# Optimization experiments

Measured on AMD Instinct MI355X. Metric: run time of the kernel, lower is better.

The kernel has to match this reference:

```python
import jax, jax.numpy as jnp
import numpy as np
import math

B = 16384
INPUT = 2048
HIDDEN = 2048
PROJ = 1024


def setup_inputs() -> dict:
    key = jax.random.key(0)
    ks = jax.random.split(key, 20)
    stdv = 1.0 / math.sqrt(PROJ)
    u = lambda k, shape: jax.random.uniform(k, shape, jnp.float32, -stdv, stdv)
    return {
        "x_t": jax.random.normal(ks[0], (B, INPUT), jnp.float32),
        "h_t": jax.random.normal(ks[1], (B, PROJ), jnp.float32),
        "c_t": jax.random.normal(ks[2], (B, HIDDEN), jnp.float32),
        "weight_if_x": u(ks[3], (INPUT, 2 * HIDDEN)),
        "weight_if_h": u(ks[4], (PROJ, 2 * HIDDEN)),
        "weight_if_c": u(ks[5], (HIDDEN, 2 * HIDDEN)),
        "bias_i": u(ks[6], (HIDDEN,)),
        "bias_f": u(ks[7], (HIDDEN,)),
        "weight_c_x": u(ks[8], (INPUT, HIDDEN)),
        "weight_c_h": u(ks[9], (PROJ, HIDDEN)),
        "bias_c": u(ks[10], (HIDDEN,)),
        "weight_o_x": u(ks[11], (INPUT, PROJ)),
        "weight_o_h": u(ks[12], (PROJ, PROJ)),
        "weight_o_c": u(ks[13], (HIDDEN, PROJ)),
        "bias_o": u(ks[14], (PROJ,)),
        "weight_r_proj": u(ks[15], (HIDDEN, PROJ)),
        "weight_r_x": u(ks[16], (INPUT, PROJ)),
    }


def reference(x_t, h_t, c_t, weight_if_x, weight_if_h, weight_if_c, bias_i, bias_f,
              weight_c_x, weight_c_h, bias_c, weight_o_x, weight_o_h, weight_o_c,
              bias_o, weight_r_proj, weight_r_x):
    # input/forget gates with peephole on c_t: [B, 2*HIDDEN]
    if_gates = x_t @ weight_if_x + h_t @ weight_if_h + c_t @ weight_if_c
    ingate, forgetgate = jnp.split(if_gates, 2, axis=-1)
    ingate = jax.nn.sigmoid(ingate + bias_i)
    forgetgate = jax.nn.sigmoid(forgetgate + bias_f)
    cellgate = jnp.tanh(x_t @ weight_c_x + h_t @ weight_c_h + bias_c)
    c_new = forgetgate * c_t + ingate * cellgate
    # output gate peeps at new cell state
    outgate = jax.nn.sigmoid(x_t @ weight_o_x + h_t @ weight_o_h + c_new @ weight_o_c + bias_o)
    r_t = jnp.tanh(c_new)
    m_t = r_t @ weight_r_proj
    # input_size != proj_size -> project x for the residual connection
    h_new = outgate * (m_t + x_t @ weight_r_x)
    return (h_new, c_new)
```

## Files before the change

### kernel.cpp

```cpp
#include <hip/hip_runtime.h>
#include <hip/hip_bf16.h>
#include <math.h>

typedef unsigned short u16;
typedef __bf16 bf16x8_t __attribute__((ext_vector_type(8)));
typedef float  f32x4_t  __attribute__((ext_vector_type(4)));
typedef float  f32x8_t  __attribute__((ext_vector_type(8)));
typedef u16    u16x4_t  __attribute__((ext_vector_type(4)));
typedef u16    u16x8_t  __attribute__((ext_vector_type(8)));

__device__ __forceinline__ u16 f2b(float f) {
  unsigned u = __builtin_bit_cast(unsigned, f);
  u += 0x7fffu + ((u >> 16) & 1u);
  return (u16)(u >> 16);
}
__device__ __forceinline__ float b2f(u16 h) {
  unsigned u = ((unsigned)h) << 16;
  return __builtin_bit_cast(float, u);
}
__device__ __forceinline__ float sigm_(float x) { return 1.0f / (1.0f + __expf(-x)); }
__device__ __forceinline__ float tanh_(float x) { return 1.0f - 2.0f / (__expf(2.0f * x) + 1.0f); }

__device__ __forceinline__ void gload16(const void* g, void* l) {
  __builtin_amdgcn_global_load_lds(
      (__attribute__((address_space(1))) void*)(g),
      (__attribute__((address_space(3))) void*)(l), 16, 0, 0);
}


__global__ void pack_act_kernel(const float* __restrict__ x, const float* __restrict__ h,
                                const float* __restrict__ c, u16* __restrict__ A1p) {
  int mb = blockIdx.x, kt = blockIdx.y, t = threadIdx.x;
  const float* src; int C, ccol;
  if (kt < 64)      { src = x; C = 2048; ccol = kt * 32; }
  else if (kt < 96) { src = h; C = 1024; ccol = (kt - 64) * 32; }
  else              { src = c; C = 2048; ccol = (kt - 96) * 32; }
  const float* s = src + (long)(mb * 256 + t) * C + ccol;
  u16* d = A1p + ((long)(mb * 160 + kt)) * 8192 + t * 8;
#pragma unroll
  for (int p = 0; p < 4; ++p) {
    f32x8_t v = *(const f32x8_t*)(s + p * 8);
    u16x8_t o;
#pragma unroll
    for (int r = 0; r < 8; ++r) o[r] = f2b(v[r]);
    *(u16x8_t*)(d + p * 2048) = o;
  }
}

__global__ void pack_w1_kernel(const float* __restrict__ w_if_x, const float* __restrict__ w_if_h,
                               const float* __restrict__ w_if_c, const float* __restrict__ w_c_x,
                               const float* __restrict__ w_c_h,  const float* __restrict__ w_o_x,
                               const float* __restrict__ w_o_h,  const float* __restrict__ w_r_x,
                               u16* __restrict__ W1tp) {
  int nb = blockIdx.x, kt = blockIdx.y, t = threadIdx.x;
  int n0g = nb * 256;
  const float* src; int N, nl, kl;
  if (n0g < 4096) {
    N = 4096; nl = n0g;
    if (kt < 64)      { src = w_if_x; kl = kt * 32; }
    else if (kt < 96) { src = w_if_h; kl = (kt - 64) * 32; }
    else              { src = w_if_c; kl = (kt - 96) * 32; }
  } else if (n0g < 6144) {
    N = 2048; nl = n0g - 4096;
    if (kt < 64)      { src = w_c_x; kl = kt * 32; }
    else if (kt < 96) { src = w_c_h; kl = (kt - 64) * 32; }
    else return;
  } else if (n0g < 7168) {
    N = 1024; nl = n0g - 6144;
    if (kt < 64)      { src = w_o_x; kl = kt * 32; }
    else if (kt < 96) { src = w_o_h; kl = (kt - 64) * 32; }
    else return;
  } else {
    N = 1024; nl = n0g - 7168;
    if (kt < 64)      { src = w_r_x; kl = kt * 32; }
    else return;
  }
  int n = nl + t;
  float tmp[32];
#pragma unroll
  for (int kk = 0; kk < 32; ++kk)
    tmp[kk] = src[(long)(kl + kk) * N + n];
  u16* d = W1tp + ((long)(nb * 160 + kt)) * 8192 + t * 8;
#pragma unroll
  for (int p = 0; p < 4; ++p) {
    u16x8_t o;
#pragma unroll
    for (int r = 0; r < 8; ++r) o[r] = f2b(tmp[p * 8 + r]);
    *(u16x8_t*)(d + p * 2048) = o;
  }
}

__global__ void pack_w2_kernel(const float* __restrict__ w_o_c,
                               const float* __restrict__ w_r_proj, u16* __restrict__ W2q) {
  int cg = blockIdx.x, kt = blockIdx.y, t = threadIdx.x;
  const float* src; int kl;
  if (kt < 64) { src = w_o_c;    kl = kt * 32; }
  else         { src = w_r_proj; kl = (kt - 64) * 32; }
  int n = cg * 128 + t;
  float tmp[32];
#pragma unroll
  for (int kk = 0; kk < 32; ++kk)
    tmp[kk] = src[(long)(kl + kk) * 1024 + n];
  u16* d = W2q + ((long)(cg * 128 + kt)) * 4096 + t * 8;
#pragma unroll
  for (int p = 0; p < 4; ++p) {
    u16x8_t o;
#pragma unroll
    for (int r = 0; r < 8; ++r) o[r] = f2b(tmp[p * 8 + r]);
    *(u16x8_t*)(d + p * 1024) = o;
  }
}

__global__ __launch_bounds__(512, 2) void gemm1_kernel(
    const u16* __restrict__ A, const u16* __restrict__ Bt, u16* __restrict__ Cout) {
  constexpr int KTF  = 160;
  constexpr int NCOL = 8192;
  constexpr int NBN  = 32;
  constexpr int SLOT = 16384;

  __shared__ u16 lds[3 * SLOT];

  int bid = blockIdx.x;
  int cpx = gridDim.x >> 3;
  bid = (bid & 7) * cpx + (bid >> 3);

  int mb = bid / NBN, nb = bid % NBN;
  int m0 = mb * 256, n0 = nb * 256;

  int NT = (nb < 16) ? 160 : ((nb < 28) ? 96 : 64);

  const int tid  = threadIdx.x;
  const int lane = tid & 63;
  const int wid  = tid >> 6;
  const int wr   = wid >> 2;
  const int wc   = wid & 3;
  const int hl16 = lane >> 4;
  const int l15  = lane & 15;

  const int dstg = tid * 8;
  const u16* pA = A  + ((long)(mb * KTF)) * 8192 + dstg;
  const u16* pB = Bt + ((long)(nb * KTF)) * 8192 + dstg;

#define STAGE(t, s) do { \
    gload16(pA + (long)(t) * 8192,        &lds[(s) * SLOT + dstg]); \
    gload16(pA + (long)(t) * 8192 + 4096, &lds[(s) * SLOT + dstg + 4096]); \
    gload16(pB + (long)(t) * 8192,        &lds[(s) * SLOT + 8192 + dstg]); \
    gload16(pB + (long)(t) * 8192 + 4096, &lds[(s) * SLOT + 8192 + dstg + 4096]); } while (0)

  const int aoff = hl16 * 2048 + (wr * 128 + l15) * 8;
  const int boff = hl16 * 2048 + (wc * 64  + l15) * 8;

  f32x4_t acc[8][4];
#pragma unroll
  for (int m = 0; m < 8; ++m)
#pragma unroll
    for (int n = 0; n < 4; ++n) acc[m][n] = (f32x4_t){0.f, 0.f, 0.f, 0.f};

  STAGE(0, 0); STAGE(1, 1);
  asm volatile("s_waitcnt vmcnt(4)" ::: "memory");
  __builtin_amdgcn_s_barrier();

  int slot = 0, s2 = 2;
  for (int t = 0; t < NT; ++t) {
    const u16* sA = &lds[slot * SLOT];
    const u16* sB = sA + 8192;
    const bool pre = (t + 2 < NT);
    if (pre) STAGE(t + 2, s2);

    bf16x8_t bv[4], av[8];
#pragma unroll
    for (int n = 0; n < 4; ++n) bv[n] = *(const bf16x8_t*)&sB[boff + n * 128];
#pragma unroll
    for (int m = 0; m < 8; ++m) av[m] = *(const bf16x8_t*)&sA[aoff + m * 128];

    __builtin_amdgcn_s_setprio(1);
#pragma unroll
    for (int m = 0; m < 8; ++m)
#pragma unroll
      for (int n = 0; n < 4; ++n)
        acc[m][n] = __builtin_amdgcn_mfma_f32_16x16x32_bf16(bv[n], av[m], acc[m][n], 0, 0, 0);
    __builtin_amdgcn_s_setprio(0);

    if (pre) asm volatile("s_waitcnt vmcnt(4)" ::: "memory");
    else     asm volatile("s_waitcnt vmcnt(0)" ::: "memory");
    __builtin_amdgcn_s_barrier();

    slot = (slot == 2) ? 0 : slot + 1;
    s2   = (s2   == 2) ? 0 : s2   + 1;
  }
#undef STAGE

  const int rowm = lane & 15;
  const int col4 = (lane >> 4) * 4;
#pragma unroll
  for (int m = 0; m < 8; ++m) {
    long rg = (long)(m0 + wr * 128 + m * 16 + rowm) * NCOL;
#pragma unroll
    for (int n = 0; n < 4; ++n) {
      int cg = n0 + wc * 64 + n * 16 + col4;
      u16x4_t o;
#pragma unroll
      for (int r = 0; r < 4; ++r) o[r] = f2b(acc[m][n][r]);
      *(u16x4_t*)&Cout[rg + cg] = o;
    }
  }
}

__global__ void pass2_kernel(const u16* __restrict__ G1, const float* __restrict__ c_t,
                             const float* __restrict__ bias_i, const float* __restrict__ bias_f,
                             const float* __restrict__ bias_c,
                             float* __restrict__ c_new_out, u16* __restrict__ A2p) {
  int mb = blockIdx.x, jg = blockIdx.y, t = threadIdx.x;
  int b = mb * 256 + t;
  int j0 = jg * 32;
  const u16* row = G1 + (long)b * 8192 + j0;
  const float* cp_p = c_t + (long)b * 2048 + j0;
  float* co_p = c_new_out + (long)b * 2048 + j0;
  u16* dc = A2p + ((long)(mb * 128 + jg)) * 8192 + t * 8;
  u16* dr = dc + (long)64 * 8192;

#pragma unroll
  for (int q = 0; q < 4; ++q) {
    u16x8_t ip = *(const u16x8_t*)(row + q * 8);
    u16x8_t fp = *(const u16x8_t*)(row + 2048 + q * 8);
    u16x8_t gp = *(const u16x8_t*)(row + 4096 + q * 8);
    f32x8_t cp = *(const f32x8_t*)(cp_p + q * 8);
    f32x8_t bi = *(const f32x8_t*)(bias_i + j0 + q * 8);
    f32x8_t bf = *(const f32x8_t*)(bias_f + j0 + q * 8);
    f32x8_t bc = *(const f32x8_t*)(bias_c + j0 + q * 8);
    f32x8_t cn;
    u16x8_t cb, rb;
#pragma unroll
    for (int r = 0; r < 8; ++r) {
      float ig = sigm_(b2f(ip[r]) + bi[r]);
      float fg = sigm_(b2f(fp[r]) + bf[r]);
      float g  = tanh_(b2f(gp[r]) + bc[r]);
      float c  = fg * cp[r] + ig * g;
      cn[r] = c;
      cb[r] = f2b(c);
      rb[r] = f2b(tanh_(c));
    }
    *(f32x8_t*)(co_p + q * 8) = cn;
    *(u16x8_t*)(dc + q * 2048) = cb;
    *(u16x8_t*)(dr + q * 2048) = rb;
  }
}

__global__ __launch_bounds__(512, 2) void gemm2h_kernel(
    const u16* __restrict__ A2p, const u16* __restrict__ W2q,
    const u16* __restrict__ G1, const float* __restrict__ bias_o,
    float* __restrict__ h_out) {
  constexpr int SLOT = 12288;

  __shared__ u16 lds[3 * SLOT];

  int bid = blockIdx.x;
  int cpx = gridDim.x >> 3;
  bid = (bid & 7) * cpx + (bid >> 3);

  int mb = bid >> 3, cg = bid & 7;
  int m0 = mb * 256, c0 = cg * 128;

  const int tid  = threadIdx.x;
  const int lane = tid & 63;
  const int wid  = tid >> 6;
  const int wr   = wid >> 1;
  const int wc   = wid & 1;
  const int hl16 = lane >> 4;
  const int l15  = lane & 15;

  const int dstg = tid * 8;
  const u16* pA = A2p + ((long)(mb * 128)) * 8192 + dstg;
  const u16* pB = W2q + ((long)(cg * 128)) * 4096 + dstg;

#define STAGE2(t, s) do { \
    gload16(pA + (long)(t) * 8192,        &lds[(s) * SLOT + dstg]); \
    gload16(pA + (long)(t) * 8192 + 4096, &lds[(s) * SLOT + dstg + 4096]); \
    gload16(pB + (long)(t) * 4096,        &lds[(s) * SLOT + 8192 + dstg]); } while (0)

  const int aoff = hl16 * 2048 + (wr * 64 + l15) * 8;
  const int boff = hl16 * 1024 + (wc * 64 + l15) * 8;

  f32x4_t acc0[4][4], acc1[4][4];
#pragma unroll
  for (int m = 0; m < 4; ++m)
#pragma unroll
    for (int n = 0; n < 4; ++n) {
      acc0[m][n] = (f32x4_t){0.f, 0.f, 0.f, 0.f};
      acc1[m][n] = (f32x4_t){0.f, 0.f, 0.f, 0.f};
    }

  STAGE2(0, 0); STAGE2(1, 1);
  asm volatile("s_waitcnt vmcnt(3)" ::: "memory");
  __builtin_amdgcn_s_barrier();

  int slot = 0, s2 = 2;
  for (int t = 0; t < 128; ++t) {
    const u16* sA = &lds[slot * SLOT];
    const u16* sB = sA + 8192;
    const bool pre = (t + 2 < 128);
    if (pre) STAGE2(t + 2, s2);

    bf16x8_t wv[4], av[4];
#pragma unroll
    for (int n = 0; n < 4; ++n) wv[n] = *(const bf16x8_t*)&sB[boff + n * 128];
#pragma unroll
    for (int m = 0; m < 4; ++m) av[m] = *(const bf16x8_t*)&sA[aoff + m * 128];

    __builtin_amdgcn_s_setprio(1);
    if (t < 64) {
#pragma unroll
      for (int m = 0; m < 4; ++m)
#pragma unroll
        for (int n = 0; n < 4; ++n)
          acc0[m][n] = __builtin_amdgcn_mfma_f32_16x16x32_bf16(wv[n], av[m], acc0[m][n], 0, 0, 0);
    } else {
#pragma unroll
      for (int m = 0; m < 4; ++m)
#pragma unroll
        for (int n = 0; n < 4; ++n)
          acc1[m][n] = __builtin_amdgcn_mfma_f32_16x16x32_bf16(wv[n], av[m], acc1[m][n], 0, 0, 0);
    }
    __builtin_amdgcn_s_setprio(0);

    if (pre) asm volatile("s_waitcnt vmcnt(3)" ::: "memory");
    else     asm volatile("s_waitcnt vmcnt(0)" ::: "memory");
    __builtin_amdgcn_s_barrier();

    slot = (slot == 2) ? 0 : slot + 1;
    s2   = (s2   == 2) ? 0 : s2   + 1;
  }
#undef STAGE2

#pragma unroll
  for (int m = 0; m < 4; ++m) {
    int row = m0 + wr * 64 + m * 16 + l15;
    const u16* g1r = G1 + (long)row * 8192;
#pragma unroll
    for (int n = 0; n < 4; ++n) {
      int jb = c0 + wc * 64 + n * 16 + 4 * hl16;
      u16x4_t og = *(const u16x4_t*)(g1r + 6144 + jb);
      u16x4_t xr = *(const u16x4_t*)(g1r + 7168 + jb);
      f32x4_t bo = *(const f32x4_t*)(bias_o + jb);
      f32x4_t h;
#pragma unroll
      for (int r = 0; r < 4; ++r) {
        float ogate = sigm_(acc0[m][n][r] + b2f(og[r]) + bo[r]);
        h[r] = ogate * (acc1[m][n][r] + b2f(xr[r]));
      }
      *(f32x4_t*)&h_out[(long)row * 1024 + jb] = h;
    }
  }
}

extern "C" void kernel_launch(void* const* d_in, const int* in_sizes, int n_in,
                              void* d_out, int out_size, void* d_ws, size_t ws_size,
                              hipStream_t stream) {
  const float* x_t      = (const float*)d_in[0];
  const float* h_t      = (const float*)d_in[1];
  const float* c_t      = (const float*)d_in[2];
  const float* w_if_x   = (const float*)d_in[3];
  const float* w_if_h   = (const float*)d_in[4];
  const float* w_if_c   = (const float*)d_in[5];
  const float* bias_i   = (const float*)d_in[6];
  const float* bias_f   = (const float*)d_in[7];
  const float* w_c_x    = (const float*)d_in[8];
  const float* w_c_h    = (const float*)d_in[9];
  const float* bias_c   = (const float*)d_in[10];
  const float* w_o_x    = (const float*)d_in[11];
  const float* w_o_h    = (const float*)d_in[12];
  const float* w_o_c    = (const float*)d_in[13];
  const float* bias_o   = (const float*)d_in[14];
  const float* w_r_proj = (const float*)d_in[15];
  const float* w_r_x    = (const float*)d_in[16];

  char* ws = (char*)d_ws;
  u16* A1p  = (u16*)(ws);
  u16* W1tp = (u16*)(ws + 167772160L);
  u16* G1   = (u16*)(ws + 251658240L);
  u16* W2q  = (u16*)(ws + 520093696L);
  u16* A2p  = (u16*)(ws);

  float* h_out = (float*)d_out;
  float* c_out = h_out + 16384L * 1024L;

  pack_act_kernel<<<dim3(64, 160), 256, 0, stream>>>(x_t, h_t, c_t, A1p);
  pack_w1_kernel<<<dim3(32, 160), 256, 0, stream>>>(w_if_x, w_if_h, w_if_c, w_c_x, w_c_h,
                                                    w_o_x, w_o_h, w_r_x, W1tp);
  pack_w2_kernel<<<dim3(8, 128), 128, 0, stream>>>(w_o_c, w_r_proj, W2q);

  gemm1_kernel<<<2048, 512, 0, stream>>>(A1p, W1tp, G1);

  pass2_kernel<<<dim3(64, 64), 256, 0, stream>>>(G1, c_t, bias_i, bias_f, bias_c, c_out, A2p);

  gemm2h_kernel<<<512, 512, 0, stream>>>(A2p, W2q, G1, bias_o, h_out);
}
```

Baseline: 1.492 ms.

## Software-pipeline LDS fragment reads with a 4-slot ring and double-buffered registers

The GEMM main loop moves from a 3-slot to a 4-slot LDS ring and issues global-to-LDS staging three tiles ahead. The loop is unrolled by two with ping-pong register fragment sets, so half of the next tile's operands are read from LDS while the current tile's MFMAs run. The goal is to hide LDS read latency behind matrix-core work instead of stalling before each MFMA burst. In exchange it uses more LDS and more registers, and the wait count still only lets one staged tile stay outstanding, which limits how much extra global-load overlap is gained.

```diff
diff --git a/kernel.cpp b/kernel.cpp
--- a/kernel.cpp
+++ b/kernel.cpp
@@ -111,6 +111,8 @@
   }
 }
 
+struct FragSet { bf16x8_t bv[4]; bf16x8_t av[4]; };
+
 __global__ __launch_bounds__(512, 2) void gemm1_kernel(
     const u16* __restrict__ A, const u16* __restrict__ Bt, u16* __restrict__ Cout) {
   constexpr int KTF  = 160;
@@ -118,7 +120,7 @@
   constexpr int NBN  = 32;
   constexpr int SLOT = 16384;
 
-  __shared__ u16 lds[3 * SLOT];
+  __shared__ u16 lds[4 * SLOT];
 
   int bid = blockIdx.x;
   int cpx = gridDim.x >> 3;
@@ -150,45 +152,64 @@
   const int aoff = hl16 * 2048 + (wr * 128 + l15) * 8;
   const int boff = hl16 * 2048 + (wc * 64  + l15) * 8;
 
+#define RD_P(S, si) do { \
+    const u16* _pb = &lds[(si) * SLOT]; \
+    const u16* _pc = _pb + 8192; \
+    _Pragma("unroll") \
+    for (int n = 0; n < 4; ++n) S.bv[n] = *(const bf16x8_t*)&_pc[boff + n * 128]; \
+    _Pragma("unroll") \
+    for (int m = 0; m < 4; ++m) S.av[m] = *(const bf16x8_t*)&_pb[aoff + m * 128]; } while (0)
+
+#define ITER(TT, P, N) do { \
+    const int _t = (TT); \
+    const u16* _sb = &lds[(_t & 3) * SLOT]; \
+    if (_t + 3 < NT) STAGE(_t + 3, (_t + 3) & 3); \
+    bf16x8_t _aq0 = *(const bf16x8_t*)&_sb[aoff + 4 * 128]; \
+    bf16x8_t _aq1 = *(const bf16x8_t*)&_sb[aoff + 5 * 128]; \
+    bf16x8_t _aq2 = *(const bf16x8_t*)&_sb[aoff + 6 * 128]; \
+    bf16x8_t _aq3 = *(const bf16x8_t*)&_sb[aoff + 7 * 128]; \
+    __builtin_amdgcn_s_setprio(1); \
+    _Pragma("unroll") \
+    for (int m = 0; m < 4; ++m) \
+      _Pragma("unroll") \
+      for (int n = 0; n < 4; ++n) \
+        acc[m][n] = __builtin_amdgcn_mfma_f32_16x16x32_bf16(P.bv[n], P.av[m], acc[m][n], 0, 0, 0); \
+    __builtin_amdgcn_s_setprio(0); \
+    if (_t + 1 < NT) RD_P(N, (_t + 1) & 3); \
+    __builtin_amdgcn_s_setprio(1); \
+    _Pragma("unroll") \
+    for (int n = 0; n < 4; ++n) { \
+      acc[4][n] = __builtin_amdgcn_mfma_f32_16x16x32_bf16(P.bv[n], _aq0, acc[4][n], 0, 0, 0); \
+      acc[5][n] = __builtin_amdgcn_mfma_f32_16x16x32_bf16(P.bv[n], _aq1, acc[5][n], 0, 0, 0); \
+      acc[6][n] = __builtin_amdgcn_mfma_f32_16x16x32_bf16(P.bv[n], _aq2, acc[6][n], 0, 0, 0); \
+      acc[7][n] = __builtin_amdgcn_mfma_f32_16x16x32_bf16(P.bv[n], _aq3, acc[7][n], 0, 0, 0); \
+    } \
+    __builtin_amdgcn_s_setprio(0); \
+    if (_t + 3 < NT) asm volatile("s_waitcnt vmcnt(4)" ::: "memory"); \
+    else             asm volatile("s_waitcnt vmcnt(0)" ::: "memory"); \
+    __builtin_amdgcn_s_barrier(); \
+  } while (0)
+
   f32x4_t acc[8][4];
 #pragma unroll
   for (int m = 0; m < 8; ++m)
 #pragma unroll
     for (int n = 0; n < 4; ++n) acc[m][n] = (f32x4_t){0.f, 0.f, 0.f, 0.f};
 
-  STAGE(0, 0); STAGE(1, 1);
+  STAGE(0, 0); STAGE(1, 1); STAGE(2, 2);
   asm volatile("s_waitcnt vmcnt(4)" ::: "memory");
   __builtin_amdgcn_s_barrier();
 
-  int slot = 0, s2 = 2;
-  for (int t = 0; t < NT; ++t) {
-    const u16* sA = &lds[slot * SLOT];
-    const u16* sB = sA + 8192;
-    const bool pre = (t + 2 < NT);
-    if (pre) STAGE(t + 2, s2);
-
-    bf16x8_t bv[4], av[8];
-#pragma unroll
-    for (int n = 0; n < 4; ++n) bv[n] = *(const bf16x8_t*)&sB[boff + n * 128];
-#pragma unroll
-    for (int m = 0; m < 8; ++m) av[m] = *(const bf16x8_t*)&sA[aoff + m * 128];
-
-    __builtin_amdgcn_s_setprio(1);
-#pragma unroll
-    for (int m = 0; m < 8; ++m)
-#pragma unroll
-      for (int n = 0; n < 4; ++n)
-        acc[m][n] = __builtin_amdgcn_mfma_f32_16x16x32_bf16(bv[n], av[m], acc[m][n], 0, 0, 0);
-    __builtin_amdgcn_s_setprio(0);
-
-    if (pre) asm volatile("s_waitcnt vmcnt(4)" ::: "memory");
-    else     asm volatile("s_waitcnt vmcnt(0)" ::: "memory");
-    __builtin_amdgcn_s_barrier();
-
-    slot = (slot == 2) ? 0 : slot + 1;
-    s2   = (s2   == 2) ? 0 : s2   + 1;
+  FragSet FA, FB;
+  RD_P(FA, 0);
+
+  for (int t = 0; t < NT; t += 2) {
+    ITER(t,     FA, FB);
+    ITER(t + 1, FB, FA);
   }
 #undef STAGE
+#undef RD_P
+#undef ITER
 
   const int rowm = lane & 15;
   const int col4 = (lane >> 4) * 4;
```

Result: no change. 1.472 ms (-1.4%).
